# Performance work log

Measured on AMD Instinct MI355X. Metric: run time of the kernel, lower is better.

The kernel has to match this reference:

```python
import jax, jax.numpy as jnp
import numpy as np

N, E, F_IN, H, L = 100000, 1600000, 256, 128, 4
ALPHA, THETA, EPS = 0.1, 0.5, 1e-5


def setup_inputs() -> dict:
    key = jax.random.key(0)
    ks = jax.random.split(key, 6)
    x = jax.random.normal(ks[0], (N, F_IN), dtype=jnp.float32)
    edge_index = jax.random.randint(ks[1], (2, E), 0, N, dtype=jnp.int32)
    lin0_w = jax.random.normal(ks[2], (F_IN, H), dtype=jnp.float32) / np.sqrt(F_IN)
    lin0_b = jnp.zeros((H,), dtype=jnp.float32)
    conv_w = jax.random.normal(ks[3], (L, H, H), dtype=jnp.float32) / np.sqrt(H)
    bn_gamma = jnp.ones((L - 1, H), dtype=jnp.float32)
    bn_beta = jnp.zeros((L - 1, H), dtype=jnp.float32)
    return {"x": x, "edge_index": edge_index, "lin0_w": lin0_w, "lin0_b": lin0_b,
            "conv_w": conv_w, "bn_gamma": bn_gamma, "bn_beta": bn_beta}


def reference(x, edge_index, lin0_w, lin0_b, conv_w, bn_gamma, bn_beta):
    n = x.shape[0]
    loops = jnp.arange(n, dtype=edge_index.dtype)
    row = jnp.concatenate([edge_index[0], loops])  # source
    col = jnp.concatenate([edge_index[1], loops])  # target
    # GCN symmetric normalization with self-loops: D^{-1/2}(A+I)D^{-1/2}
    deg = jax.ops.segment_sum(jnp.ones_like(col, dtype=x.dtype), col, num_segments=n)
    dinv = jnp.where(deg > 0, jax.lax.rsqrt(deg), 0.0)
    norm = (dinv[row] * dinv[col])[:, None]  # [E+N, 1]

    def prop(h):  # sparse aggregation: out[c] += norm * h[r]
        return jax.ops.segment_sum(h[row] * norm, col, num_segments=n)

    # GCNConv input layer
    z = prop(x @ lin0_w) + lin0_b
    x0 = z
    for i in range(L):
        h = prop(z)
        beta = float(np.log(THETA / (i + 1) + 1.0))
        s = (1.0 - ALPHA) * h + ALPHA * x0          # identity mapping to initial features
        z = (1.0 - beta) * s + beta * (s @ conv_w[i])  # shared_weights GCN2Conv
        if i < L - 1:
            mu = jnp.mean(z, axis=0)
            var = jnp.mean((z - mu) ** 2, axis=0)
            z = (z - mu) * jax.lax.rsqrt(var + EPS) * bn_gamma[i] + bn_beta[i]
            z = jax.nn.relu(z)
    return z
```

## Files before the change

kernel.cpp:

```cpp
#include <hip/hip_runtime.h>
#include <hip/hip_bf16.h>
#include <math.h>

#define H 128
#define EPS_BN 1e-5f
#define RSTATS 16

typedef __attribute__((ext_vector_type(8))) short short8;
typedef __attribute__((ext_vector_type(4))) float f32x4;

__device__ __forceinline__ float bf2f(ushort u){
  union { float f; uint v; } x; x.v = ((uint)u) << 16; return x.f;
}
__device__ __forceinline__ ushort f2bf(float f){
  union { float f; uint v; } x; x.f = f;
  uint v = x.v;
  uint r = v + 0x7fff + ((v >> 16) & 1);
  return (ushort)(r >> 16);
}

__device__ __forceinline__ void acc8(float* a, uint4 v, float wt){
  a[0] += wt*bf2f((ushort)(v.x & 0xffff)); a[1] += wt*bf2f((ushort)(v.x >> 16));
  a[2] += wt*bf2f((ushort)(v.y & 0xffff)); a[3] += wt*bf2f((ushort)(v.y >> 16));
  a[4] += wt*bf2f((ushort)(v.z & 0xffff)); a[5] += wt*bf2f((ushort)(v.z >> 16));
  a[6] += wt*bf2f((ushort)(v.w & 0xffff)); a[7] += wt*bf2f((ushort)(v.w >> 16));
}
__device__ __forceinline__ void acc8bn(float* a, uint4 v, float wt,
                                       const float* sc, const float* sh){
  float z[8] = { bf2f((ushort)(v.x & 0xffff)), bf2f((ushort)(v.x >> 16)),
                 bf2f((ushort)(v.y & 0xffff)), bf2f((ushort)(v.y >> 16)),
                 bf2f((ushort)(v.z & 0xffff)), bf2f((ushort)(v.z >> 16)),
                 bf2f((ushort)(v.w & 0xffff)), bf2f((ushort)(v.w >> 16)) };
  #pragma unroll
  for (int j = 0; j < 8; ++j){
    float y = fmaf(z[j], sc[j], sh[j]);
    y = fmaxf(y, 0.f);
    a[j] += wt*y;
  }
}


__global__ void k_count(const int* __restrict__ col, int E, int* __restrict__ cnt){
  int i = blockIdx.x*blockDim.x + threadIdx.x;
  if (i < E) atomicAdd(&cnt[col[i]], 1);
}

__global__ void k_dinv(const int* __restrict__ cnt, float* __restrict__ dinv, int n){
  int i = blockIdx.x*blockDim.x + threadIdx.x;
  if (i < n) dinv[i] = rsqrtf((float)cnt[i] + 1.0f);
}

__global__ void k_scan1(const int* __restrict__ cnt, int* __restrict__ off,
                        int* __restrict__ bsum, int n){
  __shared__ int s[1024];
  int t = threadIdx.x;
  int i = blockIdx.x*1024 + t;
  int v = (i < n) ? cnt[i] : 0;
  s[t] = v; __syncthreads();
  for (int d = 1; d < 1024; d <<= 1){
    int x = (t >= d) ? s[t-d] : 0;
    __syncthreads();
    s[t] += x;
    __syncthreads();
  }
  if (i < n) off[i] = s[t] - v;
  if (t == 1023) bsum[blockIdx.x] = s[1023];
}

__global__ void k_scan2(int* bsum, int nb){
  int l = threadIdx.x;
  int carry = 0;
  for (int b0 = 0; b0 < nb; b0 += 64){
    int i = b0 + l;
    int orig = (i < nb) ? bsum[i] : 0;
    int v = orig;
    #pragma unroll
    for (int d = 1; d < 64; d <<= 1){
      int x = __shfl_up(v, d);
      if (l >= d) v += x;
    }
    if (i < nb) bsum[i] = carry + v - orig;
    carry += __shfl(v, 63);
  }
}

__global__ void k_scan3(int* __restrict__ off, int* __restrict__ cursor,
                        const int* __restrict__ bsum, int n, int Etot){
  int i = blockIdx.x*blockDim.x + threadIdx.x;
  if (i < n){ int o = off[i] + bsum[i >> 10]; off[i] = o; cursor[i] = o; }
  if (i == 0) off[n] = Etot;
}

__global__ void k_fill(const int* __restrict__ row, const int* __restrict__ col, int E,
                       const float* __restrict__ dinv, int* __restrict__ cursor,
                       uint2* __restrict__ edge){
  int i = blockIdx.x*blockDim.x + threadIdx.x;
  if (i < E){
    int c = col[i], r = row[i];
    int p = atomicAdd(&cursor[c], 1);
    edge[p] = make_uint2((uint)r, __float_as_uint(dinv[r]*dinv[c]));
  }
}


__global__ void k_prepw(const float* __restrict__ lin0_w, const float* __restrict__ conv_w,
                        ushort* __restrict__ lin0T, ushort* __restrict__ WpT,
                        float b0, float b1, float b2, float b3){
  int i = blockIdx.x*blockDim.x + threadIdx.x;
  if (i < 128*256){
    int nn = i >> 8, k = i & 255;
    lin0T[i] = f2bf(lin0_w[k*128 + nn]);
  } else if (i < 128*256 + 4*128*128){
    int j = i - 128*256;
    int ll = j >> 14, rc = j & 16383;
    int nn = rc >> 7, k = rc & 127;
    float beta = (ll==0)?b0:(ll==1)?b1:(ll==2)?b2:b3;
    float v = beta * conv_w[ll*16384 + k*128 + nn];
    if (k == nn) v += 1.0f - beta;
    WpT[j] = f2bf(v);
  }
}


__global__ __launch_bounds__(256) void k_prop0(
    const ushort* __restrict__ h, const int* __restrict__ off,
    const uint2* __restrict__ edge, const float* __restrict__ dinv,
    const float* __restrict__ bias,
    ushort* __restrict__ z, ushort* __restrict__ x0, int n){
  int g = blockIdx.x*blockDim.x + threadIdx.x;
  int node = g >> 6;
  if (node >= n) return;
  int l = g & 63, lr = l & 15, q = l >> 4;
  int e0 = off[node], e1 = off[node+1];
  float a[8];
  #pragma unroll
  for (int j = 0; j < 8; ++j) a[j] = 0.f;
  int e = e0 + q;
  for (; e + 4 < e1; e += 8){
    uint2 edA = edge[e];
    uint2 edB = edge[e+4];
    uint4 vA = *(const uint4*)(h + (size_t)edA.x*H + lr*8);
    uint4 vB = *(const uint4*)(h + (size_t)edB.x*H + lr*8);
    acc8(a, vA, __uint_as_float(edA.y));
    acc8(a, vB, __uint_as_float(edB.y));
  }
  if (e < e1){
    uint2 ed = edge[e];
    uint4 v = *(const uint4*)(h + (size_t)ed.x*H + lr*8);
    acc8(a, v, __uint_as_float(ed.y));
  }
  if (q == 0){
    float wc = dinv[node]; wc *= wc;
    uint4 v = *(const uint4*)(h + (size_t)node*H + lr*8);
    acc8(a, v, wc);
  }
  #pragma unroll
  for (int j = 0; j < 8; ++j){
    a[j] += __shfl(a[j], l ^ 16);
    a[j] += __shfl(a[j], l ^ 32);
  }
  if (q == 0){
    float4 b0 = *(const float4*)(bias + lr*8);
    float4 b1 = *(const float4*)(bias + lr*8 + 4);
    uint4 pk;
    pk.x = (uint)f2bf(a[0]+b0.x) | ((uint)f2bf(a[1]+b0.y) << 16);
    pk.y = (uint)f2bf(a[2]+b0.z) | ((uint)f2bf(a[3]+b0.w) << 16);
    pk.z = (uint)f2bf(a[4]+b1.x) | ((uint)f2bf(a[5]+b1.y) << 16);
    pk.w = (uint)f2bf(a[6]+b1.z) | ((uint)f2bf(a[7]+b1.w) << 16);
    size_t o = (size_t)node*H + lr*8;
    *(uint4*)(z  + o) = pk;
    *(uint4*)(x0 + o) = pk;
  }
}


template<bool BNIN, bool STATS, bool OUTF32>
__global__ __launch_bounds__(256) void k_layer(
    const ushort* __restrict__ zin, const ushort* __restrict__ x0,
    const int* __restrict__ off, const uint2* __restrict__ edge,
    const float* __restrict__ dinv, const ushort* __restrict__ BT,
    const float* __restrict__ scsh,
    void* __restrict__ zout, float* __restrict__ stats, int n)
{
  __shared__ ushort Sm[32*128];
  int t = threadIdx.x;
  int w = t >> 6, l = t & 63;
  int lr = l & 15, q = l >> 4;
  int base = blockIdx.x * 32;

  float sc[8], sh[8];
  if (BNIN){
    #pragma unroll
    for (int j = 0; j < 8; ++j){
      sc[j] = scsh[lr*8 + j];
      sh[j] = scsh[128 + lr*8 + j];
    }
  }

  for (int nd = 0; nd < 8; ++nd){
    int node = base + w*8 + nd;
    float a[8];
    #pragma unroll
    for (int j = 0; j < 8; ++j) a[j] = 0.f;
    if (node < n){
      int e0 = off[node], e1 = off[node+1];
      int e = e0 + q;
      for (; e + 4 < e1; e += 8){
        uint2 edA = edge[e];
        uint2 edB = edge[e+4];
        uint4 vA = *(const uint4*)(zin + (size_t)edA.x*H + lr*8);
        uint4 vB = *(const uint4*)(zin + (size_t)edB.x*H + lr*8);
        float wA = __uint_as_float(edA.y);
        float wB = __uint_as_float(edB.y);
        if (BNIN){ acc8bn(a, vA, wA, sc, sh); acc8bn(a, vB, wB, sc, sh); }
        else     { acc8(a, vA, wA);           acc8(a, vB, wB); }
      }
      if (e < e1){
        uint2 ed = edge[e];
        uint4 v = *(const uint4*)(zin + (size_t)ed.x*H + lr*8);
        float wt = __uint_as_float(ed.y);
        if (BNIN) acc8bn(a, v, wt, sc, sh); else acc8(a, v, wt);
      }
      if (q == 0){
        float wc = dinv[node]; wc *= wc;
        uint4 v = *(const uint4*)(zin + (size_t)node*H + lr*8);
        if (BNIN) acc8bn(a, v, wc, sc, sh); else acc8(a, v, wc);
      }
    }
    #pragma unroll
    for (int j = 0; j < 8; ++j){
      a[j] += __shfl(a[j], l ^ 16);
      a[j] += __shfl(a[j], l ^ 32);
    }
    if (q == 0){
      int row = w*8 + nd;
      uint4 pk = make_uint4(0u,0u,0u,0u);
      if (node < n){
        uint4 xv = *(const uint4*)(x0 + (size_t)node*H + lr*8);
        float s0 = 0.9f*a[0] + 0.1f*bf2f((ushort)(xv.x & 0xffff));
        float s1 = 0.9f*a[1] + 0.1f*bf2f((ushort)(xv.x >> 16));
        float s2 = 0.9f*a[2] + 0.1f*bf2f((ushort)(xv.y & 0xffff));
        float s3 = 0.9f*a[3] + 0.1f*bf2f((ushort)(xv.y >> 16));
        float s4 = 0.9f*a[4] + 0.1f*bf2f((ushort)(xv.z & 0xffff));
        float s5 = 0.9f*a[5] + 0.1f*bf2f((ushort)(xv.z >> 16));
        float s6 = 0.9f*a[6] + 0.1f*bf2f((ushort)(xv.w & 0xffff));
        float s7 = 0.9f*a[7] + 0.1f*bf2f((ushort)(xv.w >> 16));
        pk.x = (uint)f2bf(s0) | ((uint)f2bf(s1) << 16);
        pk.y = (uint)f2bf(s2) | ((uint)f2bf(s3) << 16);
        pk.z = (uint)f2bf(s4) | ((uint)f2bf(s5) << 16);
        pk.w = (uint)f2bf(s6) | ((uint)f2bf(s7) << 16);
      }
      *(uint4*)(&Sm[row*128 + ((lr ^ (row & 15))*8)]) = pk;
    }
  }

  short8 bfr[2][4];
  #pragma unroll
  for (int c = 0; c < 2; ++c)
    #pragma unroll
    for (int ks = 0; ks < 4; ++ks)
      bfr[c][ks] = *(const short8*)(BT + (size_t)(w*32 + c*16 + lr)*H + ks*32 + q*8);

  __syncthreads();

  f32x4 acc[2][2];
  #pragma unroll
  for (int rt = 0; rt < 2; ++rt){
    acc[rt][0] = (f32x4){0.f,0.f,0.f,0.f};
    acc[rt][1] = (f32x4){0.f,0.f,0.f,0.f};
  }
  #pragma unroll
  for (int rt = 0; rt < 2; ++rt){
    int row = rt*16 + lr;
    #pragma unroll
    for (int ks = 0; ks < 4; ++ks){
      short8 af = *(const short8*)(&Sm[row*128 + (((ks*4 + q) ^ (row & 15))*8)]);
      acc[rt][0] = __builtin_amdgcn_mfma_f32_16x16x32_bf16(af, bfr[0][ks], acc[rt][0], 0,0,0);
      acc[rt][1] = __builtin_amdgcn_mfma_f32_16x16x32_bf16(af, bfr[1][ks], acc[rt][1], 0,0,0);
    }
  }

  #pragma unroll
  for (int rt = 0; rt < 2; ++rt){
    #pragma unroll
    for (int c = 0; c < 2; ++c){
      #pragma unroll
      for (int j = 0; j < 4; ++j){
        int row = base + rt*16 + q*4 + j;
        float v = acc[rt][c][j];
        if (OUTF32){
          if (row < n)
            ((float*)zout)[(size_t)row*H + w*32 + c*16 + lr] = v;
        } else {
          float other = __shfl(v, l ^ 1);
          if (!(lr & 1) && row < n){
            uint pk = (uint)f2bf(v) | ((uint)f2bf(other) << 16);
            ((uint*)zout)[(size_t)row*64 + w*16 + c*8 + (lr >> 1)] = pk;
          }
        }
      }
    }
  }
  if (STATS){
    #pragma unroll
    for (int c = 0; c < 2; ++c){
      float sv = 0.f, sq = 0.f;
      #pragma unroll
      for (int rt = 0; rt < 2; ++rt)
        #pragma unroll
        for (int j = 0; j < 4; ++j){
          float v = acc[rt][c][j];
          sv += v; sq += v*v;
        }
      sv += __shfl(sv, l ^ 16); sv += __shfl(sv, l ^ 32);
      sq += __shfl(sq, l ^ 16); sq += __shfl(sq, l ^ 32);
      if (q == 0){
        float* st = stats + (size_t)(blockIdx.x & (RSTATS-1))*256;
        atomicAdd(&st[w*32 + c*16 + lr], sv);
        atomicAdd(&st[128 + w*32 + c*16 + lr], sq);
      }
    }
  }
}


__global__ void k_bnfinal(const float* __restrict__ stats, const float* __restrict__ gamma,
                          const float* __restrict__ beta, float* __restrict__ scsh,
                          float inv_n){
  int f = threadIdx.x;
  float s = 0.f, s2 = 0.f;
  for (int r = 0; r < RSTATS; ++r){
    s  += stats[r*256 + f];
    s2 += stats[r*256 + 128 + f];
  }
  float mu  = s * inv_n;
  float var = s2 * inv_n - mu*mu;
  float sc  = rsqrtf(var + EPS_BN) * gamma[f];
  scsh[f]       = sc;
  scsh[128 + f] = beta[f] - mu*sc;
}


__global__ __launch_bounds__(256) void k_gemm0(
    const float* __restrict__ Af, const ushort* __restrict__ BT,
    ushort* __restrict__ Cb, int n){
  const int K = 256;
  __shared__ ushort As[64*32];
  __shared__ ushort Bs[128*32];
  int t = threadIdx.x;
  int br = blockIdx.x * 64;
  int w = t >> 6, l = t & 63;
  int lr = l & 15, lk = l >> 4;
  int swz = (lr >> 1) & 3;

  f32x4 acc[8];
  #pragma unroll
  for (int i = 0; i < 8; ++i) acc[i] = (f32x4){0.f,0.f,0.f,0.f};

  int sar = t >> 2;
  int sab = t & 3;
  int sa_off = sar*32 + ((sab ^ ((sar>>1)&3))*8);

  for (int k0 = 0; k0 < K; k0 += 32){
    int grow = br + sar;
    float4 v0 = make_float4(0.f,0.f,0.f,0.f), v1 = v0;
    if (grow < n){
      v0 = *(const float4*)(Af + (size_t)grow*K + k0 + sab*8);
      v1 = *(const float4*)(Af + (size_t)grow*K + k0 + sab*8 + 4);
    }
    ushort tmp[8] = {f2bf(v0.x),f2bf(v0.y),f2bf(v0.z),f2bf(v0.w),
                     f2bf(v1.x),f2bf(v1.y),f2bf(v1.z),f2bf(v1.w)};
    *(uint4*)(&As[sa_off]) = *(const uint4*)tmp;
    #pragma unroll
    for (int i = 0; i < 2; ++i){
      int qq = t + i*256;
      int nrow = qq >> 2, bb = qq & 3;
      uint4 v = *(const uint4*)(BT + (size_t)nrow*K + k0 + bb*8);
      *(uint4*)(&Bs[nrow*32 + ((bb ^ ((nrow>>1)&3))*8)]) = v;
    }
    __syncthreads();
    short8 af = *(const short8*)(&As[(w*16+lr)*32 + ((lk ^ swz)*8)]);
    #pragma unroll
    for (int tn = 0; tn < 8; ++tn){
      short8 bfv = *(const short8*)(&Bs[(tn*16+lr)*32 + ((lk ^ swz)*8)]);
      acc[tn] = __builtin_amdgcn_mfma_f32_16x16x32_bf16(af, bfv, acc[tn], 0, 0, 0);
    }
    __syncthreads();
  }
  int orow = br + w*16 + lk*4;
  #pragma unroll
  for (int tn = 0; tn < 8; ++tn){
    #pragma unroll
    for (int j = 0; j < 4; ++j){
      float mine  = acc[tn][j];
      float other = __shfl(mine, l ^ 1);
      if (!(l & 1) && (orow + j) < n){
        uint pk = (uint)f2bf(mine) | ((uint)f2bf(other) << 16);
        ((uint*)Cb)[(size_t)(orow+j)*64 + tn*8 + (lr >> 1)] = pk;
      }
    }
  }
}


extern "C" void kernel_launch(void* const* d_in, const int* in_sizes, int n_in,
                              void* d_out, int out_size, void* d_ws, size_t ws_size,
                              hipStream_t stream){
  const float* x        = (const float*)d_in[0];
  const int*   ei       = (const int*)  d_in[1];
  const float* lin0_w   = (const float*)d_in[2];
  const float* lin0_b   = (const float*)d_in[3];
  const float* conv_w   = (const float*)d_in[4];
  const float* bn_gamma = (const float*)d_in[5];
  const float* bn_beta  = (const float*)d_in[6];
  float* out = (float*)d_out;

  int N = in_sizes[0] / 256;
  int E = in_sizes[1] / 2;
  const int* row = ei;
  const int* col = ei + E;

  char* ws = (char*)d_ws;
  size_t p = 0;
  auto alloc = [&](size_t bytes)->char*{
    char* r = ws + p; p = (p + bytes + 255) & ~(size_t)255; return r;
  };
  int*    cnt    = (int*)   alloc((size_t)N*4);
  int*    off    = (int*)   alloc((size_t)(N+1)*4);
  int*    cursor = (int*)   alloc((size_t)N*4);
  float*  dinv   = (float*) alloc((size_t)N*4);
  int*    bsum   = (int*)   alloc(512*4);
  uint2*  edge   = (uint2*) alloc((size_t)E*8);
  ushort* zb     = (ushort*)alloc((size_t)N*H*2);
  ushort* sb     = (ushort*)alloc((size_t)N*H*2);
  ushort* x0b    = (ushort*)alloc((size_t)N*H*2);
  ushort* lin0T  = (ushort*)alloc(128*256*2);
  ushort* WpT    = (ushort*)alloc(4*128*128*2);
  float*  stats  = (float*) alloc(RSTATS*256*4);
  float*  scsh   = (float*) alloc(2*128*4);

  float betas[4];
  for (int i = 0; i < 4; ++i) betas[i] = logf(0.5f/(float)(i+1) + 1.0f);
  float inv_n = 1.0f/(float)N;

  hipMemsetAsync(cnt, 0, (size_t)N*4, stream);
  k_count<<<(E+255)/256, 256, 0, stream>>>(col, E, cnt);
  k_dinv <<<(N+255)/256, 256, 0, stream>>>(cnt, dinv, N);
  int nb = (N + 1023)/1024;
  k_scan1<<<nb, 1024, 0, stream>>>(cnt, off, bsum, N);
  k_scan2<<<1, 64, 0, stream>>>(bsum, nb);
  k_scan3<<<(N+255)/256, 256, 0, stream>>>(off, cursor, bsum, N, E);
  k_fill <<<(E+255)/256, 256, 0, stream>>>(row, col, E, dinv, cursor, edge);

  k_prepw<<<(128*256 + 4*128*128 + 255)/256, 256, 0, stream>>>(
      lin0_w, conv_w, lin0T, WpT, betas[0], betas[1], betas[2], betas[3]);

  int gemm_blocks = (N + 63)/64;
  int lay_blocks  = (N + 31)/32;
  int prop_blocks = ((N*64) + 255)/256;

  k_gemm0<<<gemm_blocks, 256, 0, stream>>>(x, lin0T, sb, N);
  k_prop0<<<prop_blocks, 256, 0, stream>>>(sb, off, edge, dinv, lin0_b, zb, x0b, N);

  hipMemsetAsync(stats, 0, RSTATS*256*4, stream);
  k_layer<false,true,false><<<lay_blocks, 256, 0, stream>>>(
      zb, x0b, off, edge, dinv, WpT + 0*128*128, nullptr, sb, stats, N);
  k_bnfinal<<<1, 128, 0, stream>>>(stats, bn_gamma + 0*H, bn_beta + 0*H, scsh, inv_n);

  hipMemsetAsync(stats, 0, RSTATS*256*4, stream);
  k_layer<true,true,false><<<lay_blocks, 256, 0, stream>>>(
      sb, x0b, off, edge, dinv, WpT + 1*128*128, scsh, zb, stats, N);
  k_bnfinal<<<1, 128, 0, stream>>>(stats, bn_gamma + 1*H, bn_beta + 1*H, scsh, inv_n);

  hipMemsetAsync(stats, 0, RSTATS*256*4, stream);
  k_layer<true,true,false><<<lay_blocks, 256, 0, stream>>>(
      zb, x0b, off, edge, dinv, WpT + 2*128*128, scsh, sb, stats, N);
  k_bnfinal<<<1, 128, 0, stream>>>(stats, bn_gamma + 2*H, bn_beta + 2*H, scsh, inv_n);

  k_layer<true,false,true><<<lay_blocks, 256, 0, stream>>>(
      sb, x0b, off, edge, dinv, WpT + 3*128*128, scsh, out, nullptr, N);
}
```

Measured before the change: 677.9 us.

## Apply BatchNorm in separate pass, unroll edge gather by four, drop duplicate z copy

Moves the BatchNorm scale/shift and ReLU out of the per-edge gather loop into a standalone elementwise kernel that rewrites the bf16 activations in place once per layer. The aggregation loops then do only plain weighted accumulation. The edge loop is unrolled to four independent gathers to keep more loads in flight. k_prop0 no longer writes a separate z copy and the first layer reads x0 directly. This trades per-edge ALU work (about 16 edges per node) for an extra read and write pass over the activation matrix per layer, plus three more launches.

```diff
diff --git a/kernel.cpp b/kernel.cpp
--- a/kernel.cpp
+++ b/kernel.cpp
@@ -24,19 +24,6 @@
   a[2] += wt*bf2f((ushort)(v.y & 0xffff)); a[3] += wt*bf2f((ushort)(v.y >> 16));
   a[4] += wt*bf2f((ushort)(v.z & 0xffff)); a[5] += wt*bf2f((ushort)(v.z >> 16));
   a[6] += wt*bf2f((ushort)(v.w & 0xffff)); a[7] += wt*bf2f((ushort)(v.w >> 16));
-}
-__device__ __forceinline__ void acc8bn(float* a, uint4 v, float wt,
-                                       const float* sc, const float* sh){
-  float z[8] = { bf2f((ushort)(v.x & 0xffff)), bf2f((ushort)(v.x >> 16)),
-                 bf2f((ushort)(v.y & 0xffff)), bf2f((ushort)(v.y >> 16)),
-                 bf2f((ushort)(v.z & 0xffff)), bf2f((ushort)(v.z >> 16)),
-                 bf2f((ushort)(v.w & 0xffff)), bf2f((ushort)(v.w >> 16)) };
-  #pragma unroll
-  for (int j = 0; j < 8; ++j){
-    float y = fmaf(z[j], sc[j], sh[j]);
-    y = fmaxf(y, 0.f);
-    a[j] += wt*y;
-  }
 }
 
 
@@ -126,7 +113,7 @@
     const ushort* __restrict__ h, const int* __restrict__ off,
     const uint2* __restrict__ edge, const float* __restrict__ dinv,
     const float* __restrict__ bias,
-    ushort* __restrict__ z, ushort* __restrict__ x0, int n){
+    ushort* __restrict__ x0, int n){
   int g = blockIdx.x*blockDim.x + threadIdx.x;
   int node = g >> 6;
   if (node >= n) return;
@@ -136,15 +123,19 @@
   #pragma unroll
   for (int j = 0; j < 8; ++j) a[j] = 0.f;
   int e = e0 + q;
-  for (; e + 4 < e1; e += 8){
-    uint2 edA = edge[e];
-    uint2 edB = edge[e+4];
+  for (; e + 12 < e1; e += 16){
+    uint2 edA = edge[e],   edB = edge[e+4];
+    uint2 edC = edge[e+8], edD = edge[e+12];
     uint4 vA = *(const uint4*)(h + (size_t)edA.x*H + lr*8);
     uint4 vB = *(const uint4*)(h + (size_t)edB.x*H + lr*8);
+    uint4 vC = *(const uint4*)(h + (size_t)edC.x*H + lr*8);
+    uint4 vD = *(const uint4*)(h + (size_t)edD.x*H + lr*8);
     acc8(a, vA, __uint_as_float(edA.y));
     acc8(a, vB, __uint_as_float(edB.y));
-  }
-  if (e < e1){
+    acc8(a, vC, __uint_as_float(edC.y));
+    acc8(a, vD, __uint_as_float(edD.y));
+  }
+  for (; e < e1; e += 4){
     uint2 ed = edge[e];
     uint4 v = *(const uint4*)(h + (size_t)ed.x*H + lr*8);
     acc8(a, v, __uint_as_float(ed.y));
@@ -167,19 +158,16 @@
     pk.y = (uint)f2bf(a[2]+b0.z) | ((uint)f2bf(a[3]+b0.w) << 16);
     pk.z = (uint)f2bf(a[4]+b1.x) | ((uint)f2bf(a[5]+b1.y) << 16);
     pk.w = (uint)f2bf(a[6]+b1.z) | ((uint)f2bf(a[7]+b1.w) << 16);
-    size_t o = (size_t)node*H + lr*8;
-    *(uint4*)(z  + o) = pk;
-    *(uint4*)(x0 + o) = pk;
-  }
-}
-
-
-template<bool BNIN, bool STATS, bool OUTF32>
+    *(uint4*)(x0 + (size_t)node*H + lr*8) = pk;
+  }
+}
+
+
+template<bool STATS, bool OUTF32>
 __global__ __launch_bounds__(256) void k_layer(
     const ushort* __restrict__ zin, const ushort* __restrict__ x0,
     const int* __restrict__ off, const uint2* __restrict__ edge,
     const float* __restrict__ dinv, const ushort* __restrict__ BT,
-    const float* __restrict__ scsh,
     void* __restrict__ zout, float* __restrict__ stats, int n)
 {
   __shared__ ushort Sm[32*128];
@@ -188,15 +176,6 @@
   int lr = l & 15, q = l >> 4;
   int base = blockIdx.x * 32;
 
-  float sc[8], sh[8];
-  if (BNIN){
-    #pragma unroll
-    for (int j = 0; j < 8; ++j){
-      sc[j] = scsh[lr*8 + j];
-      sh[j] = scsh[128 + lr*8 + j];
-    }
-  }
-
   for (int nd = 0; nd < 8; ++nd){
     int node = base + w*8 + nd;
     float a[8];
@@ -205,26 +184,27 @@
     if (node < n){
       int e0 = off[node], e1 = off[node+1];
       int e = e0 + q;
-      for (; e + 4 < e1; e += 8){
-        uint2 edA = edge[e];
-        uint2 edB = edge[e+4];
+      for (; e + 12 < e1; e += 16){
+        uint2 edA = edge[e],   edB = edge[e+4];
+        uint2 edC = edge[e+8], edD = edge[e+12];
         uint4 vA = *(const uint4*)(zin + (size_t)edA.x*H + lr*8);
         uint4 vB = *(const uint4*)(zin + (size_t)edB.x*H + lr*8);
-        float wA = __uint_as_float(edA.y);
-        float wB = __uint_as_float(edB.y);
-        if (BNIN){ acc8bn(a, vA, wA, sc, sh); acc8bn(a, vB, wB, sc, sh); }
-        else     { acc8(a, vA, wA);           acc8(a, vB, wB); }
-      }
-      if (e < e1){
+        uint4 vC = *(const uint4*)(zin + (size_t)edC.x*H + lr*8);
+        uint4 vD = *(const uint4*)(zin + (size_t)edD.x*H + lr*8);
+        acc8(a, vA, __uint_as_float(edA.y));
+        acc8(a, vB, __uint_as_float(edB.y));
+        acc8(a, vC, __uint_as_float(edC.y));
+        acc8(a, vD, __uint_as_float(edD.y));
+      }
+      for (; e < e1; e += 4){
         uint2 ed = edge[e];
         uint4 v = *(const uint4*)(zin + (size_t)ed.x*H + lr*8);
-        float wt = __uint_as_float(ed.y);
-        if (BNIN) acc8bn(a, v, wt, sc, sh); else acc8(a, v, wt);
+        acc8(a, v, __uint_as_float(ed.y));
       }
       if (q == 0){
         float wc = dinv[node]; wc *= wc;
         uint4 v = *(const uint4*)(zin + (size_t)node*H + lr*8);
-        if (BNIN) acc8bn(a, v, wc, sc, sh); else acc8(a, v, wc);
+        acc8(a, v, wc);
       }
     }
     #pragma unroll
@@ -338,6 +318,26 @@
   float sc  = rsqrtf(var + EPS_BN) * gamma[f];
   scsh[f]       = sc;
   scsh[128 + f] = beta[f] - mu*sc;
+}
+
+
+__global__ __launch_bounds__(256) void k_bnapply(
+    uint4* __restrict__ z, const float* __restrict__ scsh, int n16){
+  int i = blockIdx.x*blockDim.x + threadIdx.x;
+  if (i >= n16) return;
+  int f8 = (i & 15) * 8;
+  uint4 v = z[i];
+  uint r[4];
+  #pragma unroll
+  for (int p = 0; p < 4; ++p){
+    uint  u  = (&v.x)[p];
+    float z0 = bf2f((ushort)(u & 0xffff));
+    float z1 = bf2f((ushort)(u >> 16));
+    float y0 = fmaxf(fmaf(z0, scsh[f8 + p*2],     scsh[128 + f8 + p*2]),     0.f);
+    float y1 = fmaxf(fmaf(z1, scsh[f8 + p*2 + 1], scsh[128 + f8 + p*2 + 1]), 0.f);
+    r[p] = (uint)f2bf(y0) | ((uint)f2bf(y1) << 16);
+  }
+  z[i] = make_uint4(r[0], r[1], r[2], r[3]);
 }
 
 
@@ -458,25 +458,29 @@
   int gemm_blocks = (N + 63)/64;
   int lay_blocks  = (N + 31)/32;
   int prop_blocks = ((N*64) + 255)/256;
+  int bn_blocks   = ((N*16) + 255)/256;
 
   k_gemm0<<<gemm_blocks, 256, 0, stream>>>(x, lin0T, sb, N);
-  k_prop0<<<prop_blocks, 256, 0, stream>>>(sb, off, edge, dinv, lin0_b, zb, x0b, N);
+  k_prop0<<<prop_blocks, 256, 0, stream>>>(sb, off, edge, dinv, lin0_b, x0b, N);
 
   hipMemsetAsync(stats, 0, RSTATS*256*4, stream);
-  k_layer<false,true,false><<<lay_blocks, 256, 0, stream>>>(
-      zb, x0b, off, edge, dinv, WpT + 0*128*128, nullptr, sb, stats, N);
+  k_layer<true,false><<<lay_blocks, 256, 0, stream>>>(
+      x0b, x0b, off, edge, dinv, WpT + 0*128*128, sb, stats, N);
   k_bnfinal<<<1, 128, 0, stream>>>(stats, bn_gamma + 0*H, bn_beta + 0*H, scsh, inv_n);
+  k_bnapply<<<bn_blocks, 256, 0, stream>>>((uint4*)sb, scsh, N*16);
 
   hipMemsetAsync(stats, 0, RSTATS*256*4, stream);
-  k_layer<true,true,false><<<lay_blocks, 256, 0, stream>>>(
-      sb, x0b, off, edge, dinv, WpT + 1*128*128, scsh, zb, stats, N);
+  k_layer<true,false><<<lay_blocks, 256, 0, stream>>>(
+      sb, x0b, off, edge, dinv, WpT + 1*128*128, zb, stats, N);
   k_bnfinal<<<1, 128, 0, stream>>>(stats, bn_gamma + 1*H, bn_beta + 1*H, scsh, inv_n);
+  k_bnapply<<<bn_blocks, 256, 0, stream>>>((uint4*)zb, scsh, N*16);
 
   hipMemsetAsync(stats, 0, RSTATS*256*4, stream);
-  k_layer<true,true,false><<<lay_blocks, 256, 0, stream>>>(
-      zb, x0b, off, edge, dinv, WpT + 2*128*128, scsh, sb, stats, N);
+  k_layer<true,false><<<lay_blocks, 256, 0, stream>>>(
+      zb, x0b, off, edge, dinv, WpT + 2*128*128, sb, stats, N);
   k_bnfinal<<<1, 128, 0, stream>>>(stats, bn_gamma + 2*H, bn_beta + 2*H, scsh, inv_n);
-
-  k_layer<true,false,true><<<lay_blocks, 256, 0, stream>>>(
-      sb, x0b, off, edge, dinv, WpT + 3*128*128, scsh, out, nullptr, N);
-}
+  k_bnapply<<<bn_blocks, 256, 0, stream>>>((uint4*)sb, scsh, N*16);
+
+  k_layer<false,true><<<lay_blocks, 256, 0, stream>>>(
+      sb, x0b, off, edge, dinv, WpT + 3*128*128, out, nullptr, N);
+}
```

New measurement: 697.3 us. +2.9%, slower.
